# Kernel optimization log

Measured on AMD Instinct MI355X. Metric: run time of the kernel, lower is better.

Reference implementation:

```python
import jax, jax.numpy as jnp
import numpy as np

HEADS = 8
DIM_HEAD = 64
EPS = 1e-5


def _inst_norm_lastdim(t):
    # torch InstanceNorm1d receives [(b h), n, d]; with affine=False it normalizes
    # over the spatial (last) dim d per (b,h,n), biased variance, eps=1e-5.
    mu = jnp.mean(t, axis=-1, keepdims=True)
    var = jnp.mean(jnp.square(t - mu), axis=-1, keepdims=True)
    return (t - mu) * jax.lax.rsqrt(var + EPS)


def setup_inputs() -> dict:
    key = jax.random.key(0)
    k1, k2, k3, k4 = jax.random.split(key, 4)
    b, n, dim = 4, 8192, 256
    inner = HEADS * DIM_HEAD  # 512
    x = jax.random.normal(k1, (b, n, dim), dtype=jnp.float32)
    Wqkv = jax.random.normal(k2, (3 * inner, dim), dtype=jnp.float32) * (1.0 / np.sqrt(dim))
    Wout = jax.random.normal(k3, (dim, inner), dtype=jnp.float32) * (1.0 / np.sqrt(inner))
    bout = jax.random.normal(k4, (dim,), dtype=jnp.float32) * 0.01
    return {"x": x, "Wqkv": Wqkv, "Wout": Wout, "bout": bout}


def reference(x, Wqkv, Wout, bout):
    b, n, dim = x.shape
    qkv = jnp.einsum('bnc,fc->bnf', x, Wqkv)  # [b, n, 3*inner]
    q, k, v = jnp.split(qkv, 3, axis=-1)
    def to_heads(t):
        return t.reshape(b, n, HEADS, DIM_HEAD).transpose(0, 2, 1, 3)  # [b,h,n,d]
    q, k, v = to_heads(q), to_heads(k), to_heads(v)
    # galerkin: instance-norm k and v
    k = _inst_norm_lastdim(k)
    v = _inst_norm_lastdim(v)
    # associative linear attention: (k^T v) then q @ dots, scaled by 1/n
    dots = jnp.einsum('bhnd,bhne->bhde', k, v)        # [b,h,d,d]
    out = jnp.einsum('bhnd,bhde->bhne', q, dots) / n  # [b,h,n,d]
    out = out.transpose(0, 2, 1, 3).reshape(b, n, HEADS * DIM_HEAD)
    return jnp.einsum('bnf,cf->bnc', out, Wout) + bout
```

## Files before the change

### kernel.cpp

```cpp
#include <hip/hip_runtime.h>
#include <hip/hip_bf16.h>

#define SEQ    8192
#define EPS    1e-5f

typedef __attribute__((ext_vector_type(4))) float f32x4;
typedef __attribute__((ext_vector_type(8))) short bf16x8;
typedef __attribute__((ext_vector_type(8))) unsigned short u16x8;

__device__ __forceinline__ unsigned short f2bu(float f) {
  __hip_bfloat16 h = __float2bfloat16(f);
  return __builtin_bit_cast(unsigned short, h);
}
__device__ __forceinline__ float b2f(unsigned short u) {
  return __bfloat162float(__builtin_bit_cast(__hip_bfloat16, u));
}

__global__ __launch_bounds__(256) void prep_kernel(const float* __restrict__ x,
                                                   const float* __restrict__ W,
                                                   unsigned short* __restrict__ xb,
                                                   unsigned short* __restrict__ wb,
                                                   unsigned short* __restrict__ wqT) {
  const int bid = blockIdx.x;
  const int t = threadIdx.x;
  if (bid < 8192) {
    const int i = bid * 256 + t;
    float4 v = reinterpret_cast<const float4*>(x)[i];
    ushort4 o;
    o.x = f2bu(v.x); o.y = f2bu(v.y); o.z = f2bu(v.z); o.w = f2bu(v.w);
    reinterpret_cast<ushort4*>(xb)[i] = o;
  } else {
    const int i = (bid - 8192) * 256 + t;
    float4 v = reinterpret_cast<const float4*>(W)[i];
    ushort4 o;
    o.x = f2bu(v.x); o.y = f2bu(v.y); o.z = f2bu(v.z); o.w = f2bu(v.w);
    reinterpret_cast<ushort4*>(wb)[i] = o;
    const int e = i * 4;
    const int f = e >> 8;
    if (f < 512) {
      const int c = e & 255;
      wqT[(size_t)(c + 0) * 512 + f] = o.x;
      wqT[(size_t)(c + 1) * 512 + f] = o.y;
      wqT[(size_t)(c + 2) * 512 + f] = o.z;
      wqT[(size_t)(c + 3) * 512 + f] = o.w;
    }
  }
}

template<int NCB, int NRP, bool PERB, bool BIAS, bool OUTF32, int LDC>
__global__ __launch_bounds__(512) void gemm_fullk(const unsigned short* __restrict__ A,
                                                  const unsigned short* __restrict__ Bw,
                                                  const float* __restrict__ bias,
                                                  void* __restrict__ Cout) {
  extern __shared__ char smem[];
  unsigned short* As = (unsigned short*)smem;
  unsigned short* Bs = (unsigned short*)(smem + 65536);
  const int lin = blockIdx.x;
  const int xcd = lin & 7;
  const int loc = lin >> 3;
  const int cb  = loc % NCB;
  const int rp  = xcd * (NRP / 8) + loc / NCB;
  const int row0 = rp * 128;
  const int col0 = cb * 128;
  const unsigned short* Bp = Bw;
  if constexpr (PERB) Bp += (size_t)(row0 >> 13) * (size_t)(LDC * 256);
  const int tid  = threadIdx.x;
  const int lane = tid & 63;
  const int wave = tid >> 6;

  {
    const int srow = tid >> 5;
    const int cb16 = (tid & 31) << 4;
#pragma unroll
    for (int it = 0; it < 8; ++it) {
      const int row = it * 16 + srow;
      const int src_cb = cb16 ^ ((row & 7) << 4);
      const unsigned short* ga = A + (size_t)(row0 + row) * 256 + (src_cb >> 1);
      __builtin_amdgcn_global_load_lds(
          (const __attribute__((address_space(1))) void*)ga,
          (__attribute__((address_space(3))) void*)(smem + it * 8192 + tid * 16), 16, 0, 0);
      const unsigned short* gb = Bp + (size_t)(col0 + row) * 256 + (src_cb >> 1);
      __builtin_amdgcn_global_load_lds(
          (const __attribute__((address_space(1))) void*)gb,
          (__attribute__((address_space(3))) void*)(smem + 65536 + it * 8192 + tid * 16), 16, 0, 0);
    }
  }
  __syncthreads();

  const int wr = (wave >> 2) << 6;
  const int wc = (wave & 3) << 5;
  f32x4 acc[4][2] = {};
#pragma unroll
  for (int ks = 0; ks < 8; ++ks) {
    bf16x8 af[4], bfr[2];
#pragma unroll
    for (int mt = 0; mt < 4; ++mt) {
      const int r = wr + mt * 16 + (lane & 15);
      const int cbyt = (ks * 64 + ((lane >> 4) << 4)) ^ ((r & 7) << 4);
      af[mt] = *reinterpret_cast<const bf16x8*>(As + r * 256 + (cbyt >> 1));
    }
#pragma unroll
    for (int nt = 0; nt < 2; ++nt) {
      const int c = wc + nt * 16 + (lane & 15);
      const int cbyt = (ks * 64 + ((lane >> 4) << 4)) ^ ((c & 7) << 4);
      bfr[nt] = *reinterpret_cast<const bf16x8*>(Bs + c * 256 + (cbyt >> 1));
    }
#pragma unroll
    for (int mt = 0; mt < 4; ++mt)
#pragma unroll
      for (int nt = 0; nt < 2; ++nt)
        acc[mt][nt] = __builtin_amdgcn_mfma_f32_16x16x32_bf16(af[mt], bfr[nt], acc[mt][nt], 0, 0, 0);
  }

  if constexpr (OUTF32) {
#pragma unroll
    for (int mt = 0; mt < 4; ++mt) {
#pragma unroll
      for (int nt = 0; nt < 2; ++nt) {
        const int colg = col0 + wc + nt * 16 + (lane & 15);
        float bv = 0.0f;
        if constexpr (BIAS) bv = bias[colg];
#pragma unroll
        for (int i = 0; i < 4; ++i) {
          const int rowg = row0 + wr + mt * 16 + ((lane >> 4) << 2) + i;
          reinterpret_cast<float*>(Cout)[(size_t)rowg * LDC + colg] = acc[mt][nt][i] + bv;
        }
      }
    }
  } else {
    __syncthreads();
    unsigned short* Ct = (unsigned short*)smem;
#pragma unroll
    for (int mt = 0; mt < 4; ++mt) {
#pragma unroll
      for (int nt = 0; nt < 2; ++nt) {
        const int lc = wc + nt * 16 + (lane & 15);
        float bv = 0.0f;
        if constexpr (BIAS) bv = bias[col0 + lc];
#pragma unroll
        for (int i = 0; i < 4; ++i) {
          const int lr = wr + mt * 16 + ((lane >> 4) << 2) + i;
          Ct[lr * 128 + lc] = f2bu(acc[mt][nt][i] + bv);
        }
      }
    }
    __syncthreads();
    const int r = tid >> 2, cs = (tid & 3) << 5;
    unsigned short* gout = (unsigned short*)Cout + (size_t)(row0 + r) * LDC + col0 + cs;
    const unsigned short* lsrc = Ct + r * 128 + cs;
#pragma unroll
    for (int i = 0; i < 4; ++i)
      *reinterpret_cast<u16x8*>(gout + i * 8) = *reinterpret_cast<const u16x8*>(lsrc + i * 8);
  }
}

template<int K, int LDA, int LDC>
__global__ __launch_bounds__(256) void gemm_kernel(const unsigned short* __restrict__ A,
                                                   const unsigned short* __restrict__ Bw,
                                                   void* __restrict__ Cout) {
  __shared__ char smem2[32768];
  unsigned short* As = (unsigned short*)smem2;
  unsigned short* Bs = (unsigned short*)(smem2 + 16384);
  const int row0 = blockIdx.y * 128;
  const int col0 = blockIdx.x * 128;
  const int tid  = threadIdx.x;
  const int lane = tid & 63;
  const int wave = tid >> 6;
  const int wr = (wave >> 1) << 6;
  const int wc = (wave & 1) << 6;
  const int srow = tid >> 3;
  const int scol = (tid & 7) << 3;
  f32x4 acc[4][4] = {};
  for (int k0 = 0; k0 < K; k0 += 64) {
#pragma unroll
    for (int it = 0; it < 4; ++it) {
      const unsigned short* ga = A + (size_t)(row0 + it * 32 + srow) * LDA + (k0 + scol);
      __builtin_amdgcn_global_load_lds(
          (const __attribute__((address_space(1))) void*)ga,
          (__attribute__((address_space(3))) void*)((char*)As + (it * 4096 + wave * 1024)), 16, 0, 0);
      const unsigned short* gb = Bw + (size_t)(col0 + it * 32 + srow) * K + (k0 + scol);
      __builtin_amdgcn_global_load_lds(
          (const __attribute__((address_space(1))) void*)gb,
          (__attribute__((address_space(3))) void*)((char*)Bs + (it * 4096 + wave * 1024)), 16, 0, 0);
    }
    __syncthreads();
#pragma unroll
    for (int ks = 0; ks < 2; ++ks) {
      bf16x8 af[4], bfr[4];
#pragma unroll
      for (int mt = 0; mt < 4; ++mt)
        af[mt] = *reinterpret_cast<const bf16x8*>(
            &As[(wr + mt * 16 + (lane & 15)) * 64 + ks * 32 + (lane >> 4) * 8]);
#pragma unroll
      for (int nt = 0; nt < 4; ++nt)
        bfr[nt] = *reinterpret_cast<const bf16x8*>(
            &Bs[(wc + nt * 16 + (lane & 15)) * 64 + ks * 32 + (lane >> 4) * 8]);
#pragma unroll
      for (int mt = 0; mt < 4; ++mt)
#pragma unroll
        for (int nt = 0; nt < 4; ++nt)
          acc[mt][nt] = __builtin_amdgcn_mfma_f32_16x16x32_bf16(af[mt], bfr[nt], acc[mt][nt], 0, 0, 0);
    }
    __syncthreads();
  }
#pragma unroll
  for (int mt = 0; mt < 4; ++mt)
#pragma unroll
    for (int nt = 0; nt < 4; ++nt) {
      const int col = col0 + wc + nt * 16 + (lane & 15);
#pragma unroll
      for (int i = 0; i < 4; ++i) {
        const int row = row0 + wr + mt * 16 + ((lane >> 4) << 2) + i;
        reinterpret_cast<unsigned short*>(Cout)[(size_t)row * LDC + col] = f2bu(acc[mt][nt][i]);
      }
    }
}

__global__ __launch_bounds__(256) void dots_kernel(const unsigned short* __restrict__ kvb,
                                                   float* __restrict__ partial) {
  const int bh = blockIdx.x;
  const int chunk = blockIdx.y;
  const int b = bh >> 3, h = bh & 7;
  const int t = threadIdx.x;
  __shared__ float lbuf[2][4360];

  const int r  = t >> 3;
  const int j  = t & 7;
  const int kv = j >> 2;
  const int jj = j & 3;
  const int dq = t & 15;
  const int eq = t >> 4;

  const size_t rowbase = (size_t)(b * SEQ + chunk * 512 + r) * 1024 + kv * 512 + h * 64 + jj * 16;
  const int lds_off = kv * 2180 + r * 68 + jj * 16;

  float acc[4][4] = {};
  u16x8 raw0, raw1;
  raw0 = *reinterpret_cast<const u16x8*>(kvb + rowbase);
  raw1 = *reinterpret_cast<const u16x8*>(kvb + rowbase + 8);

  int p = 0;
  {
    float x[16];
#pragma unroll
    for (int i = 0; i < 8; ++i) { x[i] = b2f(raw0[i]); x[8 + i] = b2f(raw1[i]); }
    float s = 0.f, s2 = 0.f;
#pragma unroll
    for (int i = 0; i < 16; ++i) { s += x[i]; s2 += x[i] * x[i]; }
    s += __shfl_xor(s, 1, 64);  s2 += __shfl_xor(s2, 1, 64);
    s += __shfl_xor(s, 2, 64);  s2 += __shfl_xor(s2, 2, 64);
    const float mean = s * (1.0f / 64.0f);
    float var = s2 * (1.0f / 64.0f) - mean * mean;
    var = var < 0.f ? 0.f : var;
    const float rs = rsqrtf(var + EPS);
    float* dst = &lbuf[0][lds_off];
#pragma unroll
    for (int i = 0; i < 4; ++i) {
      f32x4 o = { (x[4*i+0]-mean)*rs, (x[4*i+1]-mean)*rs, (x[4*i+2]-mean)*rs, (x[4*i+3]-mean)*rs };
      *reinterpret_cast<f32x4*>(dst + 4 * i) = o;
    }
  }

  for (int sIt = 0; sIt < 16; ++sIt) {
    const bool more = (sIt + 1) < 16;
    if (more) {
      const unsigned short* src = kvb + rowbase + (size_t)(sIt + 1) * 32 * 1024;
      raw0 = *reinterpret_cast<const u16x8*>(src);
      raw1 = *reinterpret_cast<const u16x8*>(src + 8);
    }
    __syncthreads();
    {
      const float* lk = &lbuf[p][0];
      const float* lv = &lbuf[p][2180];
#pragma unroll 4
      for (int rr = 0; rr < 32; ++rr) {
        f32x4 kf = *reinterpret_cast<const f32x4*>(lk + rr * 68 + dq * 4);
        f32x4 vf = *reinterpret_cast<const f32x4*>(lv + rr * 68 + eq * 4);
#pragma unroll
        for (int i = 0; i < 4; ++i)
#pragma unroll
          for (int jx = 0; jx < 4; ++jx)
            acc[i][jx] = fmaf(kf[i], vf[jx], acc[i][jx]);
      }
    }
    if (more) {
      float x[16];
#pragma unroll
      for (int i = 0; i < 8; ++i) { x[i] = b2f(raw0[i]); x[8 + i] = b2f(raw1[i]); }
      float s = 0.f, s2 = 0.f;
#pragma unroll
      for (int i = 0; i < 16; ++i) { s += x[i]; s2 += x[i] * x[i]; }
      s += __shfl_xor(s, 1, 64);  s2 += __shfl_xor(s2, 1, 64);
      s += __shfl_xor(s, 2, 64);  s2 += __shfl_xor(s2, 2, 64);
      const float mean = s * (1.0f / 64.0f);
      float var = s2 * (1.0f / 64.0f) - mean * mean;
      var = var < 0.f ? 0.f : var;
      const float rs = rsqrtf(var + EPS);
      float* dst = &lbuf[p ^ 1][lds_off];
#pragma unroll
      for (int i = 0; i < 4; ++i) {
        f32x4 o = { (x[4*i+0]-mean)*rs, (x[4*i+1]-mean)*rs, (x[4*i+2]-mean)*rs, (x[4*i+3]-mean)*rs };
        *reinterpret_cast<f32x4*>(dst + 4 * i) = o;
      }
    }
    p ^= 1;
  }

  float* pp = partial + ((size_t)(chunk * 32 + bh) << 12) + (size_t)(dq * 4) * 64 + eq * 4;
#pragma unroll
  for (int i = 0; i < 4; ++i) {
    f32x4 o = { acc[i][0], acc[i][1], acc[i][2], acc[i][3] };
    *reinterpret_cast<f32x4*>(pp + i * 64) = o;
  }
}

__global__ __launch_bounds__(256) void reduce_kernel(const float* __restrict__ partial,
                                                     float* __restrict__ dots) {
  const int i = blockIdx.x * 256 + threadIdx.x;
  f32x4 s = {};
#pragma unroll
  for (int c = 0; c < 16; ++c)
    s += reinterpret_cast<const f32x4*>(partial)[(size_t)c * 32768 + i];
  reinterpret_cast<f32x4*>(dots)[i] = s;
}

__global__ __launch_bounds__(512) void m2_kernel(const float* __restrict__ dots,
                                                 const float* __restrict__ Wout,
                                                 unsigned short* __restrict__ M2) {
  const int b = blockIdx.x;
  const int c = blockIdx.y;
  const int t = threadIdx.x;
  __shared__ float wrow[512];
  wrow[t] = Wout[(size_t)c * 512 + t];
  __syncthreads();
  const int h = t >> 6, d = t & 63;
  const float* dp = dots + (size_t)(b * 8 + h) * 4096 + (size_t)d * 64;
  float s = 0.0f;
#pragma unroll 8
  for (int e = 0; e < 64; ++e) s += dp[e] * wrow[(h << 6) + e];
  M2[((size_t)b * 256 + c) * 512 + t] = f2bu(s * (1.0f / 8192.0f));
}

extern "C" void kernel_launch(void* const* d_in, const int* in_sizes, int n_in,
                              void* d_out, int out_size, void* d_ws, size_t ws_size,
                              hipStream_t stream) {
  const float* x    = (const float*)d_in[0];
  const float* Wqkv = (const float*)d_in[1];
  const float* Wout = (const float*)d_in[2];
  const float* bout = (const float*)d_in[3];
  char* ws = (char*)d_ws;
  unsigned short* xb    = (unsigned short*)(ws);
  unsigned short* wqkvb = (unsigned short*)(ws + 16777216);
  unsigned short* wqT   = (unsigned short*)(ws + 17563648);
  unsigned short* kvb   = (unsigned short*)(ws + 17825792);
  float*          part  = (float*)         (ws + 84934656);
  float*          dots  = (float*)         (ws + 93323264);
  unsigned short* m2    = (unsigned short*)(ws + 93847552);
  unsigned short* w3    = (unsigned short*)(ws + 94896128);

  hipFuncSetAttribute((const void*)gemm_fullk<8, 256, false, false, false, 1024>,
                      hipFuncAttributeMaxDynamicSharedMemorySize, 131072);
  hipFuncSetAttribute((const void*)gemm_fullk<2, 256, true, true, true, 256>,
                      hipFuncAttributeMaxDynamicSharedMemorySize, 131072);

  prep_kernel<<<dim3(8576), 256, 0, stream>>>(x, Wqkv, xb, wqkvb, wqT);
  gemm_fullk<8, 256, false, false, false, 1024><<<dim3(2048), 512, 131072, stream>>>(
      xb, wqkvb + (size_t)512 * 256, nullptr, kvb);
  dots_kernel<<<dim3(32, 16), 256, 0, stream>>>(kvb, part);
  reduce_kernel<<<dim3(128), 256, 0, stream>>>(part, dots);
  m2_kernel<<<dim3(4, 256), 512, 0, stream>>>(dots, Wout, m2);
  gemm_kernel<512, 512, 256><<<dim3(2, 8), 256, 0, stream>>>(m2, wqT, w3);
  gemm_fullk<2, 256, true, true, true, 256><<<dim3(512), 512, 131072, stream>>>(
      xb, w3, bout, d_out);
}
```

Before: 220.6 us.

## Fuse K/V projection GEMM with instance norm and k^T v partial dots

Replaces the separate K/V projection GEMM, which wrote a 64 MB bf16 kv buffer, and the dots kernel with one kernel per (batch, head, chunk). It computes K and V for 64-row slabs with MFMA, instance-normalises them in LDS and accumulates k^T v partials directly. This removes the large intermediate write and read. The output GEMM is also rewritten as a smaller-tile, K-looped kernel with static LDS and more blocks. The fused kernel uses only 512 blocks with about 135 KB of LDS each and a scalar FMA dots loop, so occupancy and latency hiding may be limited.

```diff
diff --git a/kernel.cpp b/kernel.cpp
--- a/kernel.cpp
+++ b/kernel.cpp
@@ -47,111 +47,177 @@
   }
 }
 
-template<int NCB, int NRP, bool PERB, bool BIAS, bool OUTF32, int LDC>
-__global__ __launch_bounds__(512) void gemm_fullk(const unsigned short* __restrict__ A,
-                                                  const unsigned short* __restrict__ Bw,
-                                                  const float* __restrict__ bias,
-                                                  void* __restrict__ Cout) {
-  extern __shared__ char smem[];
-  unsigned short* As = (unsigned short*)smem;
-  unsigned short* Bs = (unsigned short*)(smem + 65536);
+#define KVD_LDS 138240
+__global__ __launch_bounds__(512) void kvdots_kernel(const unsigned short* __restrict__ xb,
+                                                     const unsigned short* __restrict__ wqkvb,
+                                                     float* __restrict__ partial) {
+  extern __shared__ char sm[];
+  unsigned short* Ws = (unsigned short*)sm;
+  unsigned short* Xs = (unsigned short*)(sm + 65536);
+  float* lk  = (float*)(sm + 98304);
+  float* lv  = (float*)(sm + 98304 + 17408);
+  float* ps  = (float*)(sm + 133120);
+  float* psq = (float*)(sm + 135168);
+  float* fin = (float*)(sm + 137216);
+
   const int lin = blockIdx.x;
-  const int xcd = lin & 7;
-  const int loc = lin >> 3;
-  const int cb  = loc % NCB;
-  const int rp  = xcd * (NRP / 8) + loc / NCB;
-  const int row0 = rp * 128;
-  const int col0 = cb * 128;
-  const unsigned short* Bp = Bw;
-  if constexpr (PERB) Bp += (size_t)(row0 >> 13) * (size_t)(LDC * 256);
-  const int tid  = threadIdx.x;
-  const int lane = tid & 63;
-  const int wave = tid >> 6;
-
-  {
-    const int srow = tid >> 5;
-    const int cb16 = (tid & 31) << 4;
-#pragma unroll
-    for (int it = 0; it < 8; ++it) {
-      const int row = it * 16 + srow;
-      const int src_cb = cb16 ^ ((row & 7) << 4);
-      const unsigned short* ga = A + (size_t)(row0 + row) * 256 + (src_cb >> 1);
-      __builtin_amdgcn_global_load_lds(
-          (const __attribute__((address_space(1))) void*)ga,
-          (__attribute__((address_space(3))) void*)(smem + it * 8192 + tid * 16), 16, 0, 0);
-      const unsigned short* gb = Bp + (size_t)(col0 + row) * 256 + (src_cb >> 1);
-      __builtin_amdgcn_global_load_lds(
-          (const __attribute__((address_space(1))) void*)gb,
-          (__attribute__((address_space(3))) void*)(smem + 65536 + it * 8192 + tid * 16), 16, 0, 0);
-    }
-  }
+  const int j   = lin & 7;
+  const int m   = lin >> 3;
+  const int h   = m & 7;
+  const int pair = j * 8 + (m >> 3);
+  const int b = pair >> 4, chunk = pair & 15;
+  const int bh = b * 8 + h;
+
+  const int t = threadIdx.x, l = t & 63, w = t >> 6;
+  const int sub  = t >> 5;
+  const int cb16 = (t & 31) << 4;
+
+#pragma unroll
+  for (int p = 0; p < 8; ++p) {
+    const int rw = p * 16 + sub;
+    const int scb = cb16 ^ ((rw & 7) << 4);
+    const int g = 512 + ((rw >> 6) << 9) + (h << 6) + (rw & 63);
+    __builtin_amdgcn_global_load_lds(
+        (const __attribute__((address_space(1))) void*)(wqkvb + (size_t)g * 256 + (scb >> 1)),
+        (__attribute__((address_space(3))) void*)(sm + p * 8192 + t * 16), 16, 0, 0);
+  }
+#pragma unroll
+  for (int p = 0; p < 4; ++p) {
+    const int rx = p * 16 + sub;
+    const int scb = cb16 ^ ((rx & 7) << 4);
+    const size_t g = (size_t)(b * SEQ + chunk * 512 + rx) * 256;
+    __builtin_amdgcn_global_load_lds(
+        (const __attribute__((address_space(1))) void*)(xb + g + (scb >> 1)),
+        (__attribute__((address_space(3))) void*)(sm + 65536 + p * 8192 + t * 16), 16, 0, 0);
+  }
+
+  const int c    = (w << 4) + (l & 15);
+  const int half = w >> 2;
+  const int d    = c & 63;
+  const int g4   = l >> 4;
+  const int dq   = t & 15;
+  const int eg   = t >> 4;
+
+  float accd[4][2] = {};
+
+  for (int s = 0; s < 8; ++s) {
+    __syncthreads();
+    f32x4 acc[4] = {};
+#pragma unroll
+    for (int ks = 0; ks < 8; ++ks) {
+      const int kb = (ks << 6) + (g4 << 4);
+      const bf16x8 bfr = *reinterpret_cast<const bf16x8*>((char*)Ws + c * 512 + (kb ^ ((c & 7) << 4)));
+#pragma unroll
+      for (int mt = 0; mt < 4; ++mt) {
+        const int r = (mt << 4) + (l & 15);
+        const bf16x8 af = *reinterpret_cast<const bf16x8*>((char*)Xs + r * 512 + (kb ^ ((r & 7) << 4)));
+        acc[mt] = __builtin_amdgcn_mfma_f32_16x16x32_bf16(af, bfr, acc[mt], 0, 0, 0);
+      }
+    }
+#pragma unroll
+    for (int mt = 0; mt < 4; ++mt) {
+#pragma unroll
+      for (int i = 0; i < 4; ++i) {
+        float a = acc[mt][i];
+        float q = a * a;
+#pragma unroll
+        for (int mk = 1; mk <= 8; mk <<= 1) {
+          a += __shfl_xor(a, mk, 64);
+          q += __shfl_xor(q, mk, 64);
+        }
+        if ((l & 15) == 0) {
+          const int r = (mt << 4) + (g4 << 2) + i;
+          ps [(w << 6) + r] = a;
+          psq[(w << 6) + r] = q;
+        }
+      }
+    }
+    __syncthreads();
+    if (t < 128) {
+      const int hf = t >> 6, r = t & 63;
+      float a = 0.f, q = 0.f;
+#pragma unroll
+      for (int w2 = 0; w2 < 4; ++w2) {
+        a += ps [(((hf << 2) + w2) << 6) + r];
+        q += psq[(((hf << 2) + w2) << 6) + r];
+      }
+      const float mean = a * (1.0f / 64.0f);
+      float var = q * (1.0f / 64.0f) - mean * mean;
+      var = var < 0.f ? 0.f : var;
+      fin[(hf << 7) + (r << 1)]     = mean;
+      fin[(hf << 7) + (r << 1) + 1] = rsqrtf(var + EPS);
+    }
+    __syncthreads();
+    {
+      float* lb = half ? lv : lk;
+#pragma unroll
+      for (int mt = 0; mt < 4; ++mt) {
+#pragma unroll
+        for (int i = 0; i < 4; ++i) {
+          const int r = (mt << 4) + (g4 << 2) + i;
+          const float mean = fin[(half << 7) + (r << 1)];
+          const float rs   = fin[(half << 7) + (r << 1) + 1];
+          lb[r * 68 + d] = (acc[mt][i] - mean) * rs;
+        }
+      }
+    }
+    __syncthreads();
+    if (s < 7) {
+#pragma unroll
+      for (int p = 0; p < 4; ++p) {
+        const int rx = p * 16 + sub;
+        const int scb = cb16 ^ ((rx & 7) << 4);
+        const size_t g = (size_t)(b * SEQ + chunk * 512 + (s + 1) * 64 + rx) * 256;
+        __builtin_amdgcn_global_load_lds(
+            (const __attribute__((address_space(1))) void*)(xb + g + (scb >> 1)),
+            (__attribute__((address_space(3))) void*)(sm + 65536 + p * 8192 + t * 16), 16, 0, 0);
+      }
+    }
+#pragma unroll 8
+    for (int rr = 0; rr < 64; ++rr) {
+      const f32x4 kf = *reinterpret_cast<const f32x4*>(lk + rr * 68 + (dq << 2));
+      const float v0 = lv[rr * 68 + (eg << 1)];
+      const float v1 = lv[rr * 68 + (eg << 1) + 1];
+#pragma unroll
+      for (int i = 0; i < 4; ++i) {
+        accd[i][0] = fmaf(kf[i], v0, accd[i][0]);
+        accd[i][1] = fmaf(kf[i], v1, accd[i][1]);
+      }
+    }
+  }
+  float* pp = partial + ((size_t)(chunk * 32 + bh) << 12) + (size_t)(dq << 2) * 64 + (eg << 1);
+#pragma unroll
+  for (int i = 0; i < 4; ++i) {
+    pp[i * 64]     = accd[i][0];
+    pp[i * 64 + 1] = accd[i][1];
+  }
+}
+
+__global__ __launch_bounds__(256) void reduce_kernel(const float* __restrict__ partial,
+                                                     float* __restrict__ dots) {
+  const int i = blockIdx.x * 256 + threadIdx.x;
+  f32x4 s = {};
+#pragma unroll
+  for (int c = 0; c < 16; ++c)
+    s += reinterpret_cast<const f32x4*>(partial)[(size_t)c * 32768 + i];
+  reinterpret_cast<f32x4*>(dots)[i] = s;
+}
+
+__global__ __launch_bounds__(512) void m2_kernel(const float* __restrict__ dots,
+                                                 const float* __restrict__ Wout,
+                                                 unsigned short* __restrict__ M2) {
+  const int b = blockIdx.x;
+  const int c = blockIdx.y;
+  const int t = threadIdx.x;
+  __shared__ float wrow[512];
+  wrow[t] = Wout[(size_t)c * 512 + t];
   __syncthreads();
-
-  const int wr = (wave >> 2) << 6;
-  const int wc = (wave & 3) << 5;
-  f32x4 acc[4][2] = {};
-#pragma unroll
-  for (int ks = 0; ks < 8; ++ks) {
-    bf16x8 af[4], bfr[2];
-#pragma unroll
-    for (int mt = 0; mt < 4; ++mt) {
-      const int r = wr + mt * 16 + (lane & 15);
-      const int cbyt = (ks * 64 + ((lane >> 4) << 4)) ^ ((r & 7) << 4);
-      af[mt] = *reinterpret_cast<const bf16x8*>(As + r * 256 + (cbyt >> 1));
-    }
-#pragma unroll
-    for (int nt = 0; nt < 2; ++nt) {
-      const int c = wc + nt * 16 + (lane & 15);
-      const int cbyt = (ks * 64 + ((lane >> 4) << 4)) ^ ((c & 7) << 4);
-      bfr[nt] = *reinterpret_cast<const bf16x8*>(Bs + c * 256 + (cbyt >> 1));
-    }
-#pragma unroll
-    for (int mt = 0; mt < 4; ++mt)
-#pragma unroll
-      for (int nt = 0; nt < 2; ++nt)
-        acc[mt][nt] = __builtin_amdgcn_mfma_f32_16x16x32_bf16(af[mt], bfr[nt], acc[mt][nt], 0, 0, 0);
-  }
-
-  if constexpr (OUTF32) {
-#pragma unroll
-    for (int mt = 0; mt < 4; ++mt) {
-#pragma unroll
-      for (int nt = 0; nt < 2; ++nt) {
-        const int colg = col0 + wc + nt * 16 + (lane & 15);
-        float bv = 0.0f;
-        if constexpr (BIAS) bv = bias[colg];
-#pragma unroll
-        for (int i = 0; i < 4; ++i) {
-          const int rowg = row0 + wr + mt * 16 + ((lane >> 4) << 2) + i;
-          reinterpret_cast<float*>(Cout)[(size_t)rowg * LDC + colg] = acc[mt][nt][i] + bv;
-        }
-      }
-    }
-  } else {
-    __syncthreads();
-    unsigned short* Ct = (unsigned short*)smem;
-#pragma unroll
-    for (int mt = 0; mt < 4; ++mt) {
-#pragma unroll
-      for (int nt = 0; nt < 2; ++nt) {
-        const int lc = wc + nt * 16 + (lane & 15);
-        float bv = 0.0f;
-        if constexpr (BIAS) bv = bias[col0 + lc];
-#pragma unroll
-        for (int i = 0; i < 4; ++i) {
-          const int lr = wr + mt * 16 + ((lane >> 4) << 2) + i;
-          Ct[lr * 128 + lc] = f2bu(acc[mt][nt][i] + bv);
-        }
-      }
-    }
-    __syncthreads();
-    const int r = tid >> 2, cs = (tid & 3) << 5;
-    unsigned short* gout = (unsigned short*)Cout + (size_t)(row0 + r) * LDC + col0 + cs;
-    const unsigned short* lsrc = Ct + r * 128 + cs;
-#pragma unroll
-    for (int i = 0; i < 4; ++i)
-      *reinterpret_cast<u16x8*>(gout + i * 8) = *reinterpret_cast<const u16x8*>(lsrc + i * 8);
-  }
+  const int h = t >> 6, d = t & 63;
+  const float* dp = dots + (size_t)(b * 8 + h) * 4096 + (size_t)d * 64;
+  float s = 0.0f;
+#pragma unroll 8
+  for (int e = 0; e < 64; ++e) s += dp[e] * wrow[(h << 6) + e];
+  M2[((size_t)b * 256 + c) * 512 + t] = f2bu(s * (1.0f / 8192.0f));
 }
 
 template<int K, int LDA, int LDC>
@@ -216,129 +282,67 @@
     }
 }
 
-__global__ __launch_bounds__(256) void dots_kernel(const unsigned short* __restrict__ kvb,
-                                                   float* __restrict__ partial) {
-  const int bh = blockIdx.x;
-  const int chunk = blockIdx.y;
-  const int b = bh >> 3, h = bh & 7;
-  const int t = threadIdx.x;
-  __shared__ float lbuf[2][4360];
-
-  const int r  = t >> 3;
-  const int j  = t & 7;
-  const int kv = j >> 2;
-  const int jj = j & 3;
-  const int dq = t & 15;
-  const int eq = t >> 4;
-
-  const size_t rowbase = (size_t)(b * SEQ + chunk * 512 + r) * 1024 + kv * 512 + h * 64 + jj * 16;
-  const int lds_off = kv * 2180 + r * 68 + jj * 16;
-
-  float acc[4][4] = {};
-  u16x8 raw0, raw1;
-  raw0 = *reinterpret_cast<const u16x8*>(kvb + rowbase);
-  raw1 = *reinterpret_cast<const u16x8*>(kvb + rowbase + 8);
-
-  int p = 0;
-  {
-    float x[16];
-#pragma unroll
-    for (int i = 0; i < 8; ++i) { x[i] = b2f(raw0[i]); x[8 + i] = b2f(raw1[i]); }
-    float s = 0.f, s2 = 0.f;
-#pragma unroll
-    for (int i = 0; i < 16; ++i) { s += x[i]; s2 += x[i] * x[i]; }
-    s += __shfl_xor(s, 1, 64);  s2 += __shfl_xor(s2, 1, 64);
-    s += __shfl_xor(s, 2, 64);  s2 += __shfl_xor(s2, 2, 64);
-    const float mean = s * (1.0f / 64.0f);
-    float var = s2 * (1.0f / 64.0f) - mean * mean;
-    var = var < 0.f ? 0.f : var;
-    const float rs = rsqrtf(var + EPS);
-    float* dst = &lbuf[0][lds_off];
-#pragma unroll
-    for (int i = 0; i < 4; ++i) {
-      f32x4 o = { (x[4*i+0]-mean)*rs, (x[4*i+1]-mean)*rs, (x[4*i+2]-mean)*rs, (x[4*i+3]-mean)*rs };
-      *reinterpret_cast<f32x4*>(dst + 4 * i) = o;
-    }
-  }
-
-  for (int sIt = 0; sIt < 16; ++sIt) {
-    const bool more = (sIt + 1) < 16;
-    if (more) {
-      const unsigned short* src = kvb + rowbase + (size_t)(sIt + 1) * 32 * 1024;
-      raw0 = *reinterpret_cast<const u16x8*>(src);
-      raw1 = *reinterpret_cast<const u16x8*>(src + 8);
-    }
-    __syncthreads();
-    {
-      const float* lk = &lbuf[p][0];
-      const float* lv = &lbuf[p][2180];
-#pragma unroll 4
-      for (int rr = 0; rr < 32; ++rr) {
-        f32x4 kf = *reinterpret_cast<const f32x4*>(lk + rr * 68 + dq * 4);
-        f32x4 vf = *reinterpret_cast<const f32x4*>(lv + rr * 68 + eq * 4);
-#pragma unroll
-        for (int i = 0; i < 4; ++i)
-#pragma unroll
-          for (int jx = 0; jx < 4; ++jx)
-            acc[i][jx] = fmaf(kf[i], vf[jx], acc[i][jx]);
-      }
-    }
-    if (more) {
-      float x[16];
-#pragma unroll
-      for (int i = 0; i < 8; ++i) { x[i] = b2f(raw0[i]); x[8 + i] = b2f(raw1[i]); }
-      float s = 0.f, s2 = 0.f;
-#pragma unroll
-      for (int i = 0; i < 16; ++i) { s += x[i]; s2 += x[i] * x[i]; }
-      s += __shfl_xor(s, 1, 64);  s2 += __shfl_xor(s2, 1, 64);
-      s += __shfl_xor(s, 2, 64);  s2 += __shfl_xor(s2, 2, 64);
-      const float mean = s * (1.0f / 64.0f);
-      float var = s2 * (1.0f / 64.0f) - mean * mean;
-      var = var < 0.f ? 0.f : var;
-      const float rs = rsqrtf(var + EPS);
-      float* dst = &lbuf[p ^ 1][lds_off];
+__global__ __launch_bounds__(256) void gemm_out(const unsigned short* __restrict__ A,
+                                                const unsigned short* __restrict__ Bw,
+                                                const float* __restrict__ bias,
+                                                float* __restrict__ C) {
+  __shared__ unsigned short As[64 * 64];
+  __shared__ unsigned short Bs[128 * 64];
+  const int lin = blockIdx.x;
+  const int xcd = lin & 7, loc = lin >> 3;
+  const int cb = loc & 1, rp = xcd * 64 + (loc >> 1);
+  const int row0 = rp * 64, col0 = cb * 128;
+  const unsigned short* Bp = Bw + (size_t)(row0 >> 13) * 65536;
+  const int t = threadIdx.x, l = t & 63, w = t >> 6;
+  const int wr = (w >> 1) * 32, wc = (w & 1) * 64;
+  f32x4 acc[2][4] = {};
+  for (int k0 = 0; k0 < 256; k0 += 64) {
+#pragma unroll
+    for (int p = 0; p < 2; ++p) {
+      const unsigned short* ga = A + (size_t)(row0 + p * 32 + (t >> 3)) * 256 + k0 + ((t & 7) << 3);
+      __builtin_amdgcn_global_load_lds(
+          (const __attribute__((address_space(1))) void*)ga,
+          (__attribute__((address_space(3))) void*)((char*)As + p * 4096 + t * 16), 16, 0, 0);
+    }
+#pragma unroll
+    for (int p = 0; p < 4; ++p) {
+      const unsigned short* gb = Bp + (size_t)(col0 + p * 32 + (t >> 3)) * 256 + k0 + ((t & 7) << 3);
+      __builtin_amdgcn_global_load_lds(
+          (const __attribute__((address_space(1))) void*)gb,
+          (__attribute__((address_space(3))) void*)((char*)Bs + p * 4096 + t * 16), 16, 0, 0);
+    }
+    __syncthreads();
+#pragma unroll
+    for (int ks = 0; ks < 2; ++ks) {
+      bf16x8 af[2], bfr[4];
+#pragma unroll
+      for (int mt = 0; mt < 2; ++mt)
+        af[mt] = *reinterpret_cast<const bf16x8*>(
+            &As[(wr + mt * 16 + (l & 15)) * 64 + ks * 32 + (l >> 4) * 8]);
+#pragma unroll
+      for (int nt = 0; nt < 4; ++nt)
+        bfr[nt] = *reinterpret_cast<const bf16x8*>(
+            &Bs[(wc + nt * 16 + (l & 15)) * 64 + ks * 32 + (l >> 4) * 8]);
+#pragma unroll
+      for (int mt = 0; mt < 2; ++mt)
+#pragma unroll
+        for (int nt = 0; nt < 4; ++nt)
+          acc[mt][nt] = __builtin_amdgcn_mfma_f32_16x16x32_bf16(af[mt], bfr[nt], acc[mt][nt], 0, 0, 0);
+    }
+    __syncthreads();
+  }
+#pragma unroll
+  for (int mt = 0; mt < 2; ++mt)
+#pragma unroll
+    for (int nt = 0; nt < 4; ++nt) {
+      const int col = col0 + wc + nt * 16 + (l & 15);
+      const float bv = bias[col];
 #pragma unroll
       for (int i = 0; i < 4; ++i) {
-        f32x4 o = { (x[4*i+0]-mean)*rs, (x[4*i+1]-mean)*rs, (x[4*i+2]-mean)*rs, (x[4*i+3]-mean)*rs };
-        *reinterpret_cast<f32x4*>(dst + 4 * i) = o;
-      }
-    }
-    p ^= 1;
-  }
-
-  float* pp = partial + ((size_t)(chunk * 32 + bh) << 12) + (size_t)(dq * 4) * 64 + eq * 4;
-#pragma unroll
-  for (int i = 0; i < 4; ++i) {
-    f32x4 o = { acc[i][0], acc[i][1], acc[i][2], acc[i][3] };
-    *reinterpret_cast<f32x4*>(pp + i * 64) = o;
-  }
-}
-
-__global__ __launch_bounds__(256) void reduce_kernel(const float* __restrict__ partial,
-                                                     float* __restrict__ dots) {
-  const int i = blockIdx.x * 256 + threadIdx.x;
-  f32x4 s = {};
-#pragma unroll
-  for (int c = 0; c < 16; ++c)
-    s += reinterpret_cast<const f32x4*>(partial)[(size_t)c * 32768 + i];
-  reinterpret_cast<f32x4*>(dots)[i] = s;
-}
-
-__global__ __launch_bounds__(512) void m2_kernel(const float* __restrict__ dots,
-                                                 const float* __restrict__ Wout,
-                                                 unsigned short* __restrict__ M2) {
-  const int b = blockIdx.x;
-  const int c = blockIdx.y;
-  const int t = threadIdx.x;
-  __shared__ float wrow[512];
-  wrow[t] = Wout[(size_t)c * 512 + t];
-  __syncthreads();
-  const int h = t >> 6, d = t & 63;
-  const float* dp = dots + (size_t)(b * 8 + h) * 4096 + (size_t)d * 64;
-  float s = 0.0f;
-#pragma unroll 8
-  for (int e = 0; e < 64; ++e) s += dp[e] * wrow[(h << 6) + e];
-  M2[((size_t)b * 256 + c) * 512 + t] = f2bu(s * (1.0f / 8192.0f));
+        const int row = row0 + wr + mt * 16 + ((l >> 4) << 2) + i;
+        C[(size_t)row * 256 + col] = acc[mt][nt][i] + bv;
+      }
+    }
 }
 
 extern "C" void kernel_launch(void* const* d_in, const int* in_sizes, int n_in,
@@ -352,24 +356,18 @@
   unsigned short* xb    = (unsigned short*)(ws);
   unsigned short* wqkvb = (unsigned short*)(ws + 16777216);
   unsigned short* wqT   = (unsigned short*)(ws + 17563648);
-  unsigned short* kvb   = (unsigned short*)(ws + 17825792);
-  float*          part  = (float*)         (ws + 84934656);
-  float*          dots  = (float*)         (ws + 93323264);
-  unsigned short* m2    = (unsigned short*)(ws + 93847552);
-  unsigned short* w3    = (unsigned short*)(ws + 94896128);
-
-  hipFuncSetAttribute((const void*)gemm_fullk<8, 256, false, false, false, 1024>,
-                      hipFuncAttributeMaxDynamicSharedMemorySize, 131072);
-  hipFuncSetAttribute((const void*)gemm_fullk<2, 256, true, true, true, 256>,
-                      hipFuncAttributeMaxDynamicSharedMemorySize, 131072);
+  float*          part  = (float*)         (ws + 17825792);
+  float*          dots  = (float*)         (ws + 26214400);
+  unsigned short* m2    = (unsigned short*)(ws + 26738688);
+  unsigned short* w3    = (unsigned short*)(ws + 27787264);
+
+  (void)hipFuncSetAttribute((const void*)kvdots_kernel,
+                            hipFuncAttributeMaxDynamicSharedMemorySize, KVD_LDS);
 
   prep_kernel<<<dim3(8576), 256, 0, stream>>>(x, Wqkv, xb, wqkvb, wqT);
-  gemm_fullk<8, 256, false, false, false, 1024><<<dim3(2048), 512, 131072, stream>>>(
-      xb, wqkvb + (size_t)512 * 256, nullptr, kvb);
-  dots_kernel<<<dim3(32, 16), 256, 0, stream>>>(kvb, part);
+  kvdots_kernel<<<dim3(512), 512, KVD_LDS, stream>>>(xb, wqkvb, part);
   reduce_kernel<<<dim3(128), 256, 0, stream>>>(part, dots);
   m2_kernel<<<dim3(4, 256), 512, 0, stream>>>(dots, Wout, m2);
   gemm_kernel<512, 512, 256><<<dim3(2, 8), 256, 0, stream>>>(m2, wqT, w3);
-  gemm_fullk<2, 256, true, true, true, 256><<<dim3(512), 512, 131072, stream>>>(
-      xb, w3, bout, d_out);
-}
+  gemm_out<<<dim3(1024), 256, 0, stream>>>(xb, w3, bout, (float*)d_out);
+}
```

New measurement: 270.9 us. 1.23x slower.
